# Performance work log

Measured on AMD Instinct MI355X. Metric: run time of the kernel, lower is better.

## Reference

```python
import jax, jax.numpy as jnp
import numpy as np

# Coarse direction groups as (dx, dy) offsets, 8 groups x 3 members.
GROUPS_DXDY = (((1, 1), (2, 2), (2, 1)), ((0, 1), (0, 2), (1, 2)),
               ((-1, 1), (-2, 2), (-1, 2)), ((1, 0), (2, 0), (2, -1)),
               ((-1, 0), (-2, 0), (-2, 1)), ((1, -1), (2, -2), (1, -2)),
               ((0, -1), (0, -2), (-1, -2)), ((-1, -1), (-2, -2), (-2, -1)))


def _group_indices():
    # 24-channel layout: all (dy, dx) in 5x5 neighborhood minus center, row-major.
    offsets_dydx = [(dy, dx) for dy in range(-2, 3) for dx in range(-2, 3)
                    if (dy, dx) != (0, 0)]
    off_to_idx = {(dx, dy): i for i, (dy, dx) in enumerate(offsets_dydx)}
    return np.array([[off_to_idx[o] for o in g] for g in GROUPS_DXDY],
                    dtype=np.int32)  # (8, 3)


GROUP_IDX = _group_indices()
NUM_FINE = 24


def setup_inputs() -> dict:
    key = jax.random.key(0)
    k1, k2 = jax.random.split(key)
    B, NC, H, W = 4, 4, 256, 256
    fine_features = jax.random.normal(k1, (B, NC * NUM_FINE, H, W), dtype=jnp.float32)
    logits = jax.random.normal(k2, (8, 3), dtype=jnp.float32)
    return {"fine_features": fine_features, "logits": logits}


def reference(fine_features, logits):
    B, C, H, W = fine_features.shape
    nc = C // NUM_FINE
    # (B, nc, 24, H, W)
    x = fine_features.reshape(B, nc, NUM_FINE, H, W)
    gi = jnp.asarray(GROUP_IDX)  # (8, 3)
    # Gather fine direction channels into (B, nc, 8, 3, H, W)
    grouped = x[:, :, gi]
    # Softmax weights over the 3-member group dim, broadcast over B, nc, H, W
    w = jax.nn.softmax(logits, axis=-1)[None, None, :, :, None, None]
    fused = (grouped * w).sum(axis=3)  # (B, nc, 8, H, W)
    return fused.reshape(B, nc * 8, H, W)
```

## Files before the change

### kernel.cpp

```cpp
#include <hip/hip_runtime.h>


#define NUM_FINE 24
#define NGROUP 8

__global__ __launch_bounds__(256) void coarse_reduce_kernel(
    const float4* __restrict__ in,
    const float*  __restrict__ logits,
    float4* __restrict__ out,
    int pix4,
    int total)
{
    __shared__ float w[NGROUP][3];
    if (threadIdx.x < NGROUP) {
        const int g = threadIdx.x;
        float a = logits[g * 3 + 0];
        float b = logits[g * 3 + 1];
        float c = logits[g * 3 + 2];
        float m = fmaxf(a, fmaxf(b, c));
        float ea = __expf(a - m), eb = __expf(b - m), ec = __expf(c - m);
        float inv = 1.0f / (ea + eb + ec);
        w[g][0] = ea * inv;
        w[g][1] = eb * inv;
        w[g][2] = ec * inv;
    }
    __syncthreads();

    int idx = blockIdx.x * blockDim.x + threadIdx.x;
    if (idx >= total) return;

    int pix   = idx & (pix4 - 1);
    int plane = idx >> 14;

    const float4* ib = in  + (size_t)plane * NUM_FINE * pix4 + pix;
    float4*       ob = out + (size_t)plane * NGROUP  * pix4 + pix;

    constexpr int gi[NGROUP][3] = {
        {17, 23, 18},
        {16, 21, 22},
        {15, 19, 20},
        {12, 13,  9},
        {11, 10, 14},
        { 8,  4,  3},
        { 7,  2,  1},
        { 6,  0,  5},
    };

#pragma unroll
    for (int g = 0; g < NGROUP; ++g) {
        const float w0 = w[g][0], w1 = w[g][1], w2 = w[g][2];
        const float4 x0 = ib[(size_t)gi[g][0] * pix4];
        const float4 x1 = ib[(size_t)gi[g][1] * pix4];
        const float4 x2 = ib[(size_t)gi[g][2] * pix4];
        float4 r;
        r.x = w0 * x0.x + w1 * x1.x + w2 * x2.x;
        r.y = w0 * x0.y + w1 * x1.y + w2 * x2.y;
        r.z = w0 * x0.z + w1 * x1.z + w2 * x2.z;
        r.w = w0 * x0.w + w1 * x1.w + w2 * x2.w;
        ob[(size_t)g * pix4] = r;
    }
}

extern "C" void kernel_launch(void* const* d_in, const int* in_sizes, int n_in,
                              void* d_out, int out_size, void* d_ws, size_t ws_size,
                              hipStream_t stream) {
    const float* in     = (const float*)d_in[0];
    const float* logits = (const float*)d_in[1];
    float* out          = (float*)d_out;

    const int pix4  = (256 * 256) / 4;
    const int total = in_sizes[0] / (NUM_FINE * 4);

    const int block = 256;
    const int grid  = (total + block - 1) / block;

    coarse_reduce_kernel<<<grid, block, 0, stream>>>(
        (const float4*)in, logits, (float4*)out, pix4, total);
}
```

Before: 26.26 us.

## Split work per group across blocks and compute softmax weights per thread

Each block now handles one (plane, group, pixel-chunk) triple. It reads only the three source channels for that group, covering two float4 per thread, where before one thread looped over all eight groups for a single pixel. The shared-memory softmax and __syncthreads are replaced by every thread computing its group's three weights in registers. Shapes are hardcoded (16 planes, 16384 float4 per plane), so the kernel no longer generalizes to other sizes, and the redundant per-thread exp work is traded for removing the barrier.

```diff
diff --git a/kernel.cpp b/kernel.cpp
--- a/kernel.cpp
+++ b/kernel.cpp
@@ -3,37 +3,17 @@
 
 #define NUM_FINE 24
 #define NGROUP 8
+#define PIX4 16384
+#define CHUNKS 32
 
 __global__ __launch_bounds__(256) void coarse_reduce_kernel(
     const float4* __restrict__ in,
     const float*  __restrict__ logits,
-    float4* __restrict__ out,
-    int pix4,
-    int total)
+    float4* __restrict__ out)
 {
-    __shared__ float w[NGROUP][3];
-    if (threadIdx.x < NGROUP) {
-        const int g = threadIdx.x;
-        float a = logits[g * 3 + 0];
-        float b = logits[g * 3 + 1];
-        float c = logits[g * 3 + 2];
-        float m = fmaxf(a, fmaxf(b, c));
-        float ea = __expf(a - m), eb = __expf(b - m), ec = __expf(c - m);
-        float inv = 1.0f / (ea + eb + ec);
-        w[g][0] = ea * inv;
-        w[g][1] = eb * inv;
-        w[g][2] = ec * inv;
-    }
-    __syncthreads();
-
-    int idx = blockIdx.x * blockDim.x + threadIdx.x;
-    if (idx >= total) return;
-
-    int pix   = idx & (pix4 - 1);
-    int plane = idx >> 14;
-
-    const float4* ib = in  + (size_t)plane * NUM_FINE * pix4 + pix;
-    float4*       ob = out + (size_t)plane * NGROUP  * pix4 + pix;
+    const int chunk = blockIdx.x & (CHUNKS - 1);
+    const int g     = (blockIdx.x >> 5) & (NGROUP - 1);
+    const int plane = blockIdx.x >> 8;
 
     constexpr int gi[NGROUP][3] = {
         {17, 23, 18},
@@ -46,18 +26,32 @@
         { 6,  0,  5},
     };
 
+    const float a = logits[g * 3 + 0];
+    const float b = logits[g * 3 + 1];
+    const float c = logits[g * 3 + 2];
+    const float m  = fmaxf(a, fmaxf(b, c));
+    const float ea = __expf(a - m), eb = __expf(b - m), ec = __expf(c - m);
+    const float inv = 1.0f / (ea + eb + ec);
+    const float w0 = ea * inv, w1 = eb * inv, w2 = ec * inv;
+
+    const int base = chunk * 512 + threadIdx.x;
+
+    const float4* i0 = in + (size_t)(plane * NUM_FINE + gi[g][0]) * PIX4 + base;
+    const float4* i1 = in + (size_t)(plane * NUM_FINE + gi[g][1]) * PIX4 + base;
+    const float4* i2 = in + (size_t)(plane * NUM_FINE + gi[g][2]) * PIX4 + base;
+    float4*       ob = out + (size_t)(plane * NGROUP + g) * PIX4 + base;
+
 #pragma unroll
-    for (int g = 0; g < NGROUP; ++g) {
-        const float w0 = w[g][0], w1 = w[g][1], w2 = w[g][2];
-        const float4 x0 = ib[(size_t)gi[g][0] * pix4];
-        const float4 x1 = ib[(size_t)gi[g][1] * pix4];
-        const float4 x2 = ib[(size_t)gi[g][2] * pix4];
+    for (int k = 0; k < 2; ++k) {
+        const float4 x0 = i0[k * 256];
+        const float4 x1 = i1[k * 256];
+        const float4 x2 = i2[k * 256];
         float4 r;
         r.x = w0 * x0.x + w1 * x1.x + w2 * x2.x;
         r.y = w0 * x0.y + w1 * x1.y + w2 * x2.y;
         r.z = w0 * x0.z + w1 * x1.z + w2 * x2.z;
         r.w = w0 * x0.w + w1 * x1.w + w2 * x2.w;
-        ob[(size_t)g * pix4] = r;
+        ob[k * 256] = r;
     }
 }
 
@@ -68,12 +62,7 @@
     const float* logits = (const float*)d_in[1];
     float* out          = (float*)d_out;
 
-    const int pix4  = (256 * 256) / 4;
-    const int total = in_sizes[0] / (NUM_FINE * 4);
-
-    const int block = 256;
-    const int grid  = (total + block - 1) / block;
-
-    coarse_reduce_kernel<<<grid, block, 0, stream>>>(
-        (const float4*)in, logits, (float4*)out, pix4, total);
+    const int grid = 16 * NGROUP * CHUNKS;
+    coarse_reduce_kernel<<<grid, 256, 0, stream>>>(
+        (const float4*)in, logits, (float4*)out);
 }
```

Result: faster. 24.52 us (median of 2 runs) (-6.6%).
